# Performance work log

Measured on AMD Instinct MI355X. Metric: run time of the kernel, lower is better.

Reference implementation:

```python
import jax, jax.numpy as jnp
import numpy as np

B, S, D = 8, 512, 768
HEADS = 16           # label_n
HD = 64              # size_per_head
NEG = 1e12


def setup_inputs() -> dict:
    key = jax.random.key(0)
    k1, k2, k3 = jax.random.split(key, 3)
    hidden = jax.random.normal(k1, (B, S, D), dtype=jnp.float32)
    token_ids = jax.random.randint(k2, (B, S), 0, 21128, dtype=jnp.int32)
    W = jax.random.normal(k3, (D, HEADS * 2 * HD), dtype=jnp.float32) * 0.02
    b = jnp.zeros((HEADS * 2 * HD,), dtype=jnp.float32)
    return {"hidden": hidden, "token_ids": token_ids, "W": W, "b": b}


def _rope(x):
    # x: [B, S, H, HD] -> RoPE-rotated, Su Jianlin interleaved convention
    d = x.shape[-1]
    inv_freq = 1.0 / (10000.0 ** (jnp.arange(0, d, 2, dtype=jnp.float32) / d))  # [d/2]
    pos = jnp.arange(x.shape[1], dtype=jnp.float32)                              # [S]
    freqs = pos[:, None] * inv_freq[None, :]                                     # [S, d/2]
    sin = jnp.repeat(jnp.sin(freqs), 2, axis=-1)[None, :, None, :]               # [1,S,1,d]
    cos = jnp.repeat(jnp.cos(freqs), 2, axis=-1)[None, :, None, :]
    x2 = jnp.stack([-x[..., 1::2], x[..., 0::2]], axis=-1).reshape(x.shape)
    return x * cos + x2 * sin


def reference(hidden, token_ids, W, b):
    # qk projection: [B,S,H,2,HD]
    qk = (hidden @ W + b).reshape(B, S, HEADS, 2, HD)
    q, k = qk[..., 0, :], qk[..., 1, :]          # [B,S,H,HD]
    q = _rope(q)
    k = _rope(k)
    # all-pairs span scores per entity head
    logits = jnp.einsum('bmhd,bnhd->bhmn', q, k) / jnp.sqrt(jnp.float32(HD))
    # padding mask from token ids (0 = pad)
    mask = (token_ids > 0).astype(logits.dtype)  # [B,S]
    logits = logits - (1.0 - mask[:, None, :, None]) * NEG
    logits = logits - (1.0 - mask[:, None, None, :]) * NEG
    # strict lower-triangular mask (spans must have start <= end)
    tril = jnp.tril(jnp.ones((S, S), dtype=logits.dtype), k=-1)
    logits = logits - tril[None, None, :, :] * NEG
    # valid-span weight mask (upper triangle incl. diag, both positions valid)
    tri_mask = (1.0 - tril)[None, None, :, :] * mask[:, None, :, None] * mask[:, None, None, :]
    return logits, tri_mask
```

## Files before the change

kernel.cpp:

```cpp
#include <hip/hip_runtime.h>
#include <hip/hip_bf16.h>
#include <cstdint>
#include <cstddef>


#define NEGV 1.0e12f

typedef short bf16x8 __attribute__((ext_vector_type(8)));
typedef float f32x4  __attribute__((ext_vector_type(4)));

static __device__ __forceinline__ short f2b(float x) {
    __hip_bfloat16 h = __float2bfloat16(x);
    union { __hip_bfloat16 h; short s; } u; u.h = h; return u.s;
}
static __device__ __forceinline__ float b2f(short s) {
    union { short s; __hip_bfloat16 h; } u; u.s = s; return __bfloat162float(u.h);
}
static __device__ __forceinline__ void gload16(const short* g, short* l) {
    __builtin_amdgcn_global_load_lds(
        (const __attribute__((address_space(1))) void*)g,
        (__attribute__((address_space(3))) void*)l, 16, 0, 0);
}

__global__ __launch_bounds__(256) void prep_kernel(const float* __restrict__ hidden,
                                                   const float* __restrict__ W,
                                                   short* __restrict__ Xb,
                                                   short* __restrict__ Wt,
                                                   float* __restrict__ SinT,
                                                   float* __restrict__ CosT) {
    __shared__ short T[64 * 68];
    int blk = blockIdx.x, tid = threadIdx.x;
    if (blk < 1536) {
        int t = blk * 256 + tid;
        const float4* hp = (const float4*)hidden;
        float4 a = hp[t * 2], c = hp[t * 2 + 1];
        bf16x8 v;
        v[0] = f2b(a.x); v[1] = f2b(a.y); v[2] = f2b(a.z); v[3] = f2b(a.w);
        v[4] = f2b(c.x); v[5] = f2b(c.y); v[6] = f2b(c.z); v[7] = f2b(c.w);
        *(bf16x8*)(Xb + t * 8) = v;
    } else if (blk < 1600) {
        int u = (blk - 1536) * 256 + tid;
        int s = u >> 5, i = u & 31;
        float ang = (float)s * exp2f(-0.4152410118609203f * (float)i);
        float sn, cs; __sincosf(ang, &sn, &cs);
        SinT[u] = sn; CosT[u] = cs;
    } else {
        int tb = blk - 1600;
        int k0 = (tb % 12) * 64, n0 = (tb / 12) * 64;
        int r = tid >> 2, cb = (tid & 3) * 4;
#pragma unroll
        for (int q = 0; q < 4; ++q) {
            int c = cb + q * 16;
            float4 v = *(const float4*)(W + (size_t)(k0 + r) * 2048 + n0 + c);
            short* tp = T + r * 68 + c;
            tp[0] = f2b(v.x); tp[1] = f2b(v.y); tp[2] = f2b(v.z); tp[3] = f2b(v.w);
        }
        __syncthreads();
        int n = tid >> 2, kc = (tid & 3) * 16;
        bf16x8 o0, o1;
#pragma unroll
        for (int j = 0; j < 8; ++j) {
            o0[j] = T[(kc + j) * 68 + n];
            o1[j] = T[(kc + 8 + j) * 68 + n];
        }
        short* wp = Wt + (size_t)(n0 + n) * 768 + k0 + kc;
        *(bf16x8*)wp = o0;
        *(bf16x8*)(wp + 8) = o1;
    }
}

__global__ __launch_bounds__(256) void gemm_rope(const short* __restrict__ A,
                                                 const short* __restrict__ Bt,
                                                 const float* __restrict__ bias,
                                                 const float* __restrict__ SinT,
                                                 const float* __restrict__ CosT,
                                                 short* __restrict__ Qb,
                                                 short* __restrict__ Kb) {
    __shared__ short As[128 * 32];
    __shared__ short Bs[128 * 32];
    const int m0 = (blockIdx.x >> 4) * 128;
    const int n0 = (blockIdx.x & 15) * 128;
    const int tid  = threadIdx.x;
    const int wave = tid >> 6, lane = tid & 63;
    const int quad = lane >> 4, r16 = lane & 15;
    const int wm = (wave >> 1) * 64, wn = (wave & 1) * 64;

    const int swc = ((lane & 3) ^ ((lane >> 3) & 3)) * 8;
    const int r0  = wave * 32 + (lane >> 2);
    const short* gA0 = A  + (size_t)(m0 + r0) * 768 + swc;
    const short* gA1 = A  + (size_t)(m0 + r0 + 16) * 768 + swc;
    const short* gB0 = Bt + (size_t)(n0 + r0) * 768 + swc;
    const short* gB1 = Bt + (size_t)(n0 + r0 + 16) * 768 + swc;
    short* lA0 = As + wave * 1024;
    short* lA1 = As + wave * 1024 + 512;
    short* lB0 = Bs + wave * 1024;
    short* lB1 = Bs + wave * 1024 + 512;

    const int sw16 = (r16 >> 1) & 3;

    f32x4 acc[4][4] = {};
    for (int k0 = 0; k0 < 768; k0 += 32) {
        __syncthreads();
        gload16(gA0 + k0, lA0);
        gload16(gA1 + k0, lA1);
        gload16(gB0 + k0, lB0);
        gload16(gB1 + k0, lB1);
        __syncthreads();

        bf16x8 af[4], bfr[4];
#pragma unroll
        for (int mi = 0; mi < 4; ++mi)
            af[mi] = *(const bf16x8*)(As + (wm + mi * 16 + r16) * 32 + (quad ^ sw16) * 8);
#pragma unroll
        for (int ni = 0; ni < 4; ++ni)
            bfr[ni] = *(const bf16x8*)(Bs + (wn + ni * 16 + r16) * 32 + (quad ^ sw16) * 8);
#pragma unroll
        for (int mi = 0; mi < 4; ++mi)
#pragma unroll
            for (int ni = 0; ni < 4; ++ni)
                acc[mi][ni] = __builtin_amdgcn_mfma_f32_16x16x32_bf16(
                    af[mi], bfr[ni], acc[mi][ni], 0, 0, 0);
    }

    const int b     = m0 >> 9;
    const int s0l   = (m0 & 511) + wm + quad * 4;
    const int h     = n0 >> 7;
    const int which = wn >> 6;
    short* dstT = (which ? Kb : Qb) + (size_t)(b * 16 + h) * 512 * 64;
    const float sgn = (r16 & 1) ? 1.0f : -1.0f;
#pragma unroll
    for (int ni = 0; ni < 4; ++ni) {
        int col = n0 + wn + ni * 16 + r16;
        float bv = bias[col];
        int d  = ni * 16 + r16;
        int ii = d >> 1;
#pragma unroll
        for (int mi = 0; mi < 4; ++mi)
#pragma unroll
            for (int r = 0; r < 4; ++r) {
                int s = s0l + mi * 16 + r;
                float v  = acc[mi][ni][r] + bv;
                float pv = __shfl_xor(v, 1);
                float sn = SinT[s * 32 + ii];
                float cs = CosT[s * 32 + ii];
                dstT[(size_t)s * 64 + d] = f2b(v * cs + sgn * pv * sn);
            }
    }
}

__global__ __launch_bounds__(256) void logits_kernel(const short* __restrict__ Qb,
                                                     const short* __restrict__ Kb,
                                                     const int* __restrict__ tok,
                                                     float* __restrict__ out,
                                                     float* __restrict__ out2) {
    __shared__ short Qs[128 * 64];
    __shared__ short Ks[128 * 64];
    __shared__ float rowNeg[128];
    __shared__ float colNeg[128];

    int blk = blockIdx.x;
    int nt = blk & 3, mt = (blk >> 2) & 3, bh = blk >> 4;
    int b = bh >> 4, h = bh & 15;
    int m0 = mt * 128, n0 = nt * 128;

    const int tid  = threadIdx.x;
    const int wave = tid >> 6, lane = tid & 63;
    const int quad = lane >> 4, r16 = lane & 15;
    const int wm = (wave >> 1) * 64, wn = (wave & 1) * 64;

    const short* gsrc = (wave < 2)
        ? Qb + ((size_t)bh * 512 + m0) * 64
        : Kb + ((size_t)bh * 512 + n0) * 64;
    short* ldst = (wave < 2) ? Qs : Ks;
    const int wv = wave & 1;
    const int gc = ((lane & 7) ^ (lane >> 3)) * 8;
    const int rl = wv * 64 + (lane >> 3);
#pragma unroll
    for (int j = 0; j < 8; ++j)
        gload16(gsrc + (rl + j * 8) * 64 + gc, ldst + wv * 4096 + j * 512);

    if (tid < 128)      rowNeg[tid]       = (tok[b * 512 + m0 + tid] > 0) ? 0.f : NEGV;
    else if (tid < 256) colNeg[tid - 128] = (tok[b * 512 + n0 + (tid - 128)] > 0) ? 0.f : NEGV;
    __syncthreads();

    const int sw8 = r16 & 7;
    f32x4 acc[4][4] = {};
#pragma unroll
    for (int kb = 0; kb < 2; ++kb) {
        bf16x8 af[4], bfr[4];
#pragma unroll
        for (int mi = 0; mi < 4; ++mi)
            af[mi] = *(const bf16x8*)(Qs + (wm + mi * 16 + r16) * 64
                                         + ((quad + kb * 4) ^ sw8) * 8);
#pragma unroll
        for (int ni = 0; ni < 4; ++ni)
            bfr[ni] = *(const bf16x8*)(Ks + (wn + ni * 16 + r16) * 64
                                          + ((quad + kb * 4) ^ sw8) * 8);
#pragma unroll
        for (int mi = 0; mi < 4; ++mi)
#pragma unroll
            for (int ni = 0; ni < 4; ++ni)
                acc[mi][ni] = __builtin_amdgcn_mfma_f32_16x16x32_bf16(
                    af[mi], bfr[ni], acc[mi][ni], 0, 0, 0);
    }

    float* obase = out + (size_t)bh * 512 * 512;
#pragma unroll
    for (int mi = 0; mi < 4; ++mi)
#pragma unroll
        for (int ni = 0; ni < 4; ++ni) {
            int n = n0 + wn + ni * 16 + r16;
            float cn = colNeg[n - n0];
#pragma unroll
            for (int r = 0; r < 4; ++r) {
                int m = m0 + wm + mi * 16 + quad * 4 + r;
                float v = acc[mi][ni][r] * 0.125f - rowNeg[m - m0] - cn
                          - ((m > n) ? NEGV : 0.0f);
                obase[(size_t)m * 512 + n] = v;
            }
        }

    if (h == 0) {
        float* o2 = out2 + (size_t)b * 512 * 512;
#pragma unroll
        for (int mi = 0; mi < 4; ++mi)
#pragma unroll
            for (int ni = 0; ni < 4; ++ni) {
                int n = n0 + wn + ni * 16 + r16;
                float mn = (colNeg[n - n0] == 0.f) ? 1.f : 0.f;
#pragma unroll
                for (int r = 0; r < 4; ++r) {
                    int m = m0 + wm + mi * 16 + quad * 4 + r;
                    float mm = (rowNeg[m - m0] == 0.f) ? 1.f : 0.f;
                    o2[(size_t)m * 512 + n] = (m > n) ? 0.f : (mm * mn);
                }
            }
    }
}

extern "C" void kernel_launch(void* const* d_in, const int* in_sizes, int n_in,
                              void* d_out, int out_size, void* d_ws, size_t ws_size,
                              hipStream_t stream) {
    const float* hidden = (const float*)d_in[0];
    const int*   tok    = (const int*)d_in[1];
    const float* W      = (const float*)d_in[2];
    const float* bias   = (const float*)d_in[3];
    float* out  = (float*)d_out;
    float* out2 = out + 33554432;

    char* ws = (char*)d_ws;
    short* Xb   = (short*)(ws);
    short* Wt   = (short*)(ws + 6291456);
    float* SinT = (float*)(ws + 9437184);
    float* CosT = (float*)(ws + 9502720);
    short* Qb   = (short*)(ws + 9568256);
    short* Kb   = (short*)(ws + 17956864);

    hipLaunchKernelGGL(prep_kernel,   dim3(1984), dim3(256), 0, stream,
                       hidden, W, Xb, Wt, SinT, CosT);
    hipLaunchKernelGGL(gemm_rope,     dim3(512),  dim3(256), 0, stream,
                       Xb, Wt, bias, SinT, CosT, Qb, Kb);
    hipLaunchKernelGGL(logits_kernel, dim3(2048), dim3(256), 0, stream,
                       Qb, Kb, tok, out, out2);
}
```

Before: 189.1 us.

## Fuse QK projection, RoPE and logits into one per-head kernel using LDS

Merges the GEMM+RoPE kernel and the logits kernel into a single kernel with one 512-thread block per (batch, head). RoPE-rotated Q and K stay in shared memory instead of going through global workspace, and one launch is removed. The valid-span mask output is now written with vector stores split across all heads. In exchange, the grid shrinks to 128 large blocks using 128KB LDS each, so fewer CUs are busy during the large output write and the GEMM phase.

```diff
diff --git a/kernel.cpp b/kernel.cpp
--- a/kernel.cpp
+++ b/kernel.cpp
@@ -12,9 +12,6 @@
 static __device__ __forceinline__ short f2b(float x) {
     __hip_bfloat16 h = __float2bfloat16(x);
     union { __hip_bfloat16 h; short s; } u; u.h = h; return u.s;
-}
-static __device__ __forceinline__ float b2f(short s) {
-    union { short s; __hip_bfloat16 h; } u; u.s = s; return __bfloat162float(u.h);
 }
 static __device__ __forceinline__ void gload16(const short* g, short* l) {
     __builtin_amdgcn_global_load_lds(
@@ -69,172 +66,158 @@
     }
 }
 
-__global__ __launch_bounds__(256) void gemm_rope(const short* __restrict__ A,
-                                                 const short* __restrict__ Bt,
-                                                 const float* __restrict__ bias,
-                                                 const float* __restrict__ SinT,
-                                                 const float* __restrict__ CosT,
-                                                 short* __restrict__ Qb,
-                                                 short* __restrict__ Kb) {
-    __shared__ short As[128 * 32];
-    __shared__ short Bs[128 * 32];
-    const int m0 = (blockIdx.x >> 4) * 128;
-    const int n0 = (blockIdx.x & 15) * 128;
-    const int tid  = threadIdx.x;
-    const int wave = tid >> 6, lane = tid & 63;
+__global__ __launch_bounds__(512) void fused_kernel(const short* __restrict__ Xb,
+                                                    const short* __restrict__ Wt,
+                                                    const float* __restrict__ bias,
+                                                    const float* __restrict__ SinT,
+                                                    const float* __restrict__ CosT,
+                                                    const int* __restrict__ tok,
+                                                    float* __restrict__ out,
+                                                    float* __restrict__ out2) {
+    __shared__ short QK[65536];
+    __shared__ float maskNeg[512];
+
+    const int bh = blockIdx.x, b = bh >> 4, h = bh & 15;
+    const int tid = threadIdx.x, wave = tid >> 6, lane = tid & 63;
     const int quad = lane >> 4, r16 = lane & 15;
-    const int wm = (wave >> 1) * 64, wn = (wave & 1) * 64;
-
-    const int swc = ((lane & 3) ^ ((lane >> 3) & 3)) * 8;
-    const int r0  = wave * 32 + (lane >> 2);
-    const short* gA0 = A  + (size_t)(m0 + r0) * 768 + swc;
-    const short* gA1 = A  + (size_t)(m0 + r0 + 16) * 768 + swc;
-    const short* gB0 = Bt + (size_t)(n0 + r0) * 768 + swc;
-    const short* gB1 = Bt + (size_t)(n0 + r0 + 16) * 768 + swc;
-    short* lA0 = As + wave * 1024;
-    short* lA1 = As + wave * 1024 + 512;
-    short* lB0 = Bs + wave * 1024;
-    short* lB1 = Bs + wave * 1024 + 512;
-
+
+    maskNeg[tid] = (tok[b * 512 + tid] > 0) ? 0.f : NEGV;
+
+    const int wm = (wave >> 1) * 128;
+    const int wn = (wave & 1) * 64;
+    short* As = QK;
+    short* Bs = QK + 16384;
+
+    const short* Ag = Xb + (size_t)b * 512 * 768;
+    const short* Bg = Wt + (size_t)h * 128 * 768;
+
+    int aRow[4], aCol[4];
+#pragma unroll
+    for (int j = 0; j < 4; ++j) {
+        int r = j * 128 + wave * 16 + (lane >> 2);
+        aRow[j] = r;
+        aCol[j] = ((lane & 3) ^ ((r >> 1) & 3)) * 8;
+    }
+    const int bR = wave * 16 + (lane >> 2);
+    const int bC = ((lane & 3) ^ ((bR >> 1) & 3)) * 8;
     const int sw16 = (r16 >> 1) & 3;
 
-    f32x4 acc[4][4] = {};
+    f32x4 acc[8][4] = {};
     for (int k0 = 0; k0 < 768; k0 += 32) {
         __syncthreads();
-        gload16(gA0 + k0, lA0);
-        gload16(gA1 + k0, lA1);
-        gload16(gB0 + k0, lB0);
-        gload16(gB1 + k0, lB1);
+#pragma unroll
+        for (int j = 0; j < 4; ++j)
+            gload16(Ag + (size_t)aRow[j] * 768 + k0 + aCol[j],
+                    As + (j * 512 + wave * 64) * 8);
+        gload16(Bg + (size_t)bR * 768 + k0 + bC, Bs + (wave * 64) * 8);
         __syncthreads();
 
-        bf16x8 af[4], bfr[4];
-#pragma unroll
-        for (int mi = 0; mi < 4; ++mi)
-            af[mi] = *(const bf16x8*)(As + (wm + mi * 16 + r16) * 32 + (quad ^ sw16) * 8);
+        bf16x8 af[8], bfr[4];
+#pragma unroll
+        for (int mi = 0; mi < 8; ++mi)
+            af[mi] = *(const bf16x8*)(As + (wm + mi * 16 + r16) * 32 + ((quad ^ sw16) * 8));
 #pragma unroll
         for (int ni = 0; ni < 4; ++ni)
-            bfr[ni] = *(const bf16x8*)(Bs + (wn + ni * 16 + r16) * 32 + (quad ^ sw16) * 8);
-#pragma unroll
-        for (int mi = 0; mi < 4; ++mi)
+            bfr[ni] = *(const bf16x8*)(Bs + (wn + ni * 16 + r16) * 32 + ((quad ^ sw16) * 8));
+#pragma unroll
+        for (int mi = 0; mi < 8; ++mi)
 #pragma unroll
             for (int ni = 0; ni < 4; ++ni)
                 acc[mi][ni] = __builtin_amdgcn_mfma_f32_16x16x32_bf16(
                     af[mi], bfr[ni], acc[mi][ni], 0, 0, 0);
     }
-
-    const int b     = m0 >> 9;
-    const int s0l   = (m0 & 511) + wm + quad * 4;
-    const int h     = n0 >> 7;
-    const int which = wn >> 6;
-    short* dstT = (which ? Kb : Qb) + (size_t)(b * 16 + h) * 512 * 64;
-    const float sgn = (r16 & 1) ? 1.0f : -1.0f;
+    __syncthreads();
+
 #pragma unroll
     for (int ni = 0; ni < 4; ++ni) {
-        int col = n0 + wn + ni * 16 + r16;
-        float bv = bias[col];
-        int d  = ni * 16 + r16;
+        int col = wn + ni * 16 + r16;
+        float bv = bias[h * 128 + col];
+        int d = col & 63;
+        short* dst = QK + ((col >> 6) ? 32768 : 0);
         int ii = d >> 1;
+        float sgn = (col & 1) ? 1.0f : -1.0f;
+        int swk = ((d >> 3) * 8) , dlo = d & 7;
+#pragma unroll
+        for (int mi = 0; mi < 8; ++mi) {
+            int mB = wm + mi * 16 + quad * 4;
+#pragma unroll
+            for (int r = 0; r < 4; ++r) {
+                int m = mB + r;
+                float v = acc[mi][ni][r] + bv;
+                float pv = __shfl_xor(v, 1);
+                float sn = SinT[m * 32 + ii];
+                float cs = CosT[m * 32 + ii];
+                dst[m * 64 + (swk ^ ((m & 7) * 8)) + dlo] = f2b(v * cs + sgn * pv * sn);
+            }
+        }
+    }
+    __syncthreads();
+
+    const int pm = wave * 64;
+    const int sw8 = r16 & 7;
+    bf16x8 qf[4][2];
+#pragma unroll
+    for (int mi = 0; mi < 4; ++mi)
+#pragma unroll
+        for (int kb = 0; kb < 2; ++kb) {
+            int rq = pm + mi * 16 + r16;
+            qf[mi][kb] = *(const bf16x8*)(QK + rq * 64 + (((quad + kb * 4) ^ sw8) * 8));
+        }
+
+    const short* Kl = QK + 32768;
+    float* obase = out + (size_t)bh * 262144;
+#pragma unroll 1
+    for (int p = 0; p < 8; ++p) {
+        int n0 = p * 64;
+        bf16x8 kf[4][2];
+#pragma unroll
+        for (int ni = 0; ni < 4; ++ni)
+#pragma unroll
+            for (int kb = 0; kb < 2; ++kb) {
+                int rk = n0 + ni * 16 + r16;
+                kf[ni][kb] = *(const bf16x8*)(Kl + rk * 64 + (((quad + kb * 4) ^ sw8) * 8));
+            }
+        f32x4 a2[4][4] = {};
+#pragma unroll
+        for (int kb = 0; kb < 2; ++kb)
+#pragma unroll
+            for (int mi = 0; mi < 4; ++mi)
+#pragma unroll
+                for (int ni = 0; ni < 4; ++ni)
+                    a2[mi][ni] = __builtin_amdgcn_mfma_f32_16x16x32_bf16(
+                        qf[mi][kb], kf[ni][kb], a2[mi][ni], 0, 0, 0);
 #pragma unroll
         for (int mi = 0; mi < 4; ++mi)
 #pragma unroll
-            for (int r = 0; r < 4; ++r) {
-                int s = s0l + mi * 16 + r;
-                float v  = acc[mi][ni][r] + bv;
-                float pv = __shfl_xor(v, 1);
-                float sn = SinT[s * 32 + ii];
-                float cs = CosT[s * 32 + ii];
-                dstT[(size_t)s * 64 + d] = f2b(v * cs + sgn * pv * sn);
-            }
-    }
-}
-
-__global__ __launch_bounds__(256) void logits_kernel(const short* __restrict__ Qb,
-                                                     const short* __restrict__ Kb,
-                                                     const int* __restrict__ tok,
-                                                     float* __restrict__ out,
-                                                     float* __restrict__ out2) {
-    __shared__ short Qs[128 * 64];
-    __shared__ short Ks[128 * 64];
-    __shared__ float rowNeg[128];
-    __shared__ float colNeg[128];
-
-    int blk = blockIdx.x;
-    int nt = blk & 3, mt = (blk >> 2) & 3, bh = blk >> 4;
-    int b = bh >> 4, h = bh & 15;
-    int m0 = mt * 128, n0 = nt * 128;
-
-    const int tid  = threadIdx.x;
-    const int wave = tid >> 6, lane = tid & 63;
-    const int quad = lane >> 4, r16 = lane & 15;
-    const int wm = (wave >> 1) * 64, wn = (wave & 1) * 64;
-
-    const short* gsrc = (wave < 2)
-        ? Qb + ((size_t)bh * 512 + m0) * 64
-        : Kb + ((size_t)bh * 512 + n0) * 64;
-    short* ldst = (wave < 2) ? Qs : Ks;
-    const int wv = wave & 1;
-    const int gc = ((lane & 7) ^ (lane >> 3)) * 8;
-    const int rl = wv * 64 + (lane >> 3);
-#pragma unroll
-    for (int j = 0; j < 8; ++j)
-        gload16(gsrc + (rl + j * 8) * 64 + gc, ldst + wv * 4096 + j * 512);
-
-    if (tid < 128)      rowNeg[tid]       = (tok[b * 512 + m0 + tid] > 0) ? 0.f : NEGV;
-    else if (tid < 256) colNeg[tid - 128] = (tok[b * 512 + n0 + (tid - 128)] > 0) ? 0.f : NEGV;
-    __syncthreads();
-
-    const int sw8 = r16 & 7;
-    f32x4 acc[4][4] = {};
-#pragma unroll
-    for (int kb = 0; kb < 2; ++kb) {
-        bf16x8 af[4], bfr[4];
-#pragma unroll
-        for (int mi = 0; mi < 4; ++mi)
-            af[mi] = *(const bf16x8*)(Qs + (wm + mi * 16 + r16) * 64
-                                         + ((quad + kb * 4) ^ sw8) * 8);
-#pragma unroll
-        for (int ni = 0; ni < 4; ++ni)
-            bfr[ni] = *(const bf16x8*)(Ks + (wn + ni * 16 + r16) * 64
-                                          + ((quad + kb * 4) ^ sw8) * 8);
-#pragma unroll
-        for (int mi = 0; mi < 4; ++mi)
-#pragma unroll
-            for (int ni = 0; ni < 4; ++ni)
-                acc[mi][ni] = __builtin_amdgcn_mfma_f32_16x16x32_bf16(
-                    af[mi], bfr[ni], acc[mi][ni], 0, 0, 0);
-    }
-
-    float* obase = out + (size_t)bh * 512 * 512;
-#pragma unroll
-    for (int mi = 0; mi < 4; ++mi)
-#pragma unroll
-        for (int ni = 0; ni < 4; ++ni) {
-            int n = n0 + wn + ni * 16 + r16;
-            float cn = colNeg[n - n0];
-#pragma unroll
-            for (int r = 0; r < 4; ++r) {
-                int m = m0 + wm + mi * 16 + quad * 4 + r;
-                float v = acc[mi][ni][r] * 0.125f - rowNeg[m - m0] - cn
-                          - ((m > n) ? NEGV : 0.0f);
-                obase[(size_t)m * 512 + n] = v;
-            }
-        }
-
-    if (h == 0) {
-        float* o2 = out2 + (size_t)b * 512 * 512;
-#pragma unroll
-        for (int mi = 0; mi < 4; ++mi)
-#pragma unroll
             for (int ni = 0; ni < 4; ++ni) {
-                int n = n0 + wn + ni * 16 + r16;
-                float mn = (colNeg[n - n0] == 0.f) ? 1.f : 0.f;
+                int n = n0 + ni * 16 + r16;
+                float cn = maskNeg[n];
 #pragma unroll
                 for (int r = 0; r < 4; ++r) {
-                    int m = m0 + wm + mi * 16 + quad * 4 + r;
-                    float mm = (rowNeg[m - m0] == 0.f) ? 1.f : 0.f;
-                    o2[(size_t)m * 512 + n] = (m > n) ? 0.f : (mm * mn);
+                    int m = pm + mi * 16 + quad * 4 + r;
+                    float v = a2[mi][ni][r] * 0.125f - maskNeg[m] - cn
+                              - ((m > n) ? NEGV : 0.0f);
+                    obase[(size_t)m * 512 + n] = v;
                 }
             }
+    }
+
+    {
+        float* o2 = out2 + (size_t)b * 262144;
+        int m = h * 32 + (tid >> 4);
+        float mm = (maskNeg[m] == 0.f) ? 1.f : 0.f;
+        int nb = (tid & 15) * 32;
+#pragma unroll
+        for (int j = 0; j < 8; ++j) {
+            f32x4 v;
+#pragma unroll
+            for (int e = 0; e < 4; ++e) {
+                int n = nb + j * 4 + e;
+                float mn = (maskNeg[n] == 0.f) ? 1.f : 0.f;
+                v[e] = (m > n) ? 0.f : (mm * mn);
+            }
+            *(f32x4*)(o2 + (size_t)m * 512 + nb + j * 4) = v;
+        }
     }
 }
 
@@ -253,13 +236,9 @@
     short* Wt   = (short*)(ws + 6291456);
     float* SinT = (float*)(ws + 9437184);
     float* CosT = (float*)(ws + 9502720);
-    short* Qb   = (short*)(ws + 9568256);
-    short* Kb   = (short*)(ws + 17956864);
-
-    hipLaunchKernelGGL(prep_kernel,   dim3(1984), dim3(256), 0, stream,
+
+    hipLaunchKernelGGL(prep_kernel,  dim3(1984), dim3(256), 0, stream,
                        hidden, W, Xb, Wt, SinT, CosT);
-    hipLaunchKernelGGL(gemm_rope,     dim3(512),  dim3(256), 0, stream,
-                       Xb, Wt, bias, SinT, CosT, Qb, Kb);
-    hipLaunchKernelGGL(logits_kernel, dim3(2048), dim3(256), 0, stream,
-                       Qb, Kb, tok, out, out2);
-}
+    hipLaunchKernelGGL(fused_kernel, dim3(128),  dim3(512), 0, stream,
+                       Xb, Wt, bias, SinT, CosT, tok, out, out2);
+}
```

Measured after the change: 200.7 us. 1.06x slower.
